# Kernel optimization log

Measured on AMD Instinct MI355X. Metric: run time of the kernel, lower is better.

## Reference

```python
import jax, jax.numpy as jnp
import numpy as np

D_MODEL = 1024
NUM_HEADS = 16
HEAD_DIM = D_MODEL // NUM_HEADS
SEQ_LEN = 2048
BATCH = 2


def setup_inputs() -> dict:
    key = jax.random.key(0)
    ks = jax.random.split(key, 8)
    s = 1.0 / np.sqrt(D_MODEL)
    x = jax.random.normal(ks[0], (BATCH, SEQ_LEN, D_MODEL), jnp.float32)
    Wq = jax.random.normal(ks[1], (D_MODEL, D_MODEL), jnp.float32) * s
    Wk = jax.random.normal(ks[2], (D_MODEL, D_MODEL), jnp.float32) * s
    Wv = jax.random.normal(ks[3], (D_MODEL, D_MODEL), jnp.float32) * s
    Wo = jax.random.normal(ks[4], (D_MODEL, D_MODEL), jnp.float32) * s
    bq = jnp.zeros((D_MODEL,), jnp.float32)
    bk = jnp.zeros((D_MODEL,), jnp.float32)
    bv = jnp.zeros((D_MODEL,), jnp.float32)
    bo = jnp.zeros((D_MODEL,), jnp.float32)
    pos_embed = jax.random.normal(ks[5], (SEQ_LEN, HEAD_DIM), jnp.float32) * (1.0 / np.sqrt(HEAD_DIM))
    alpha = jnp.ones((NUM_HEADS, 1, 1), jnp.float32)
    beta = jnp.zeros((NUM_HEADS, 1, 1), jnp.float32)
    mask = jnp.ones((BATCH, SEQ_LEN), jnp.int32)
    return {"x": x, "mask": mask, "Wq": Wq, "bq": bq, "Wk": Wk, "bk": bk,
            "Wv": Wv, "bv": bv, "Wo": Wo, "bo": bo,
            "pos_embed": pos_embed, "alpha": alpha, "beta": beta}


def reference(x, mask, Wq, bq, Wk, bk, Wv, bv, Wo, bo, pos_embed, alpha, beta):
    B, S, _ = x.shape
    H, Dh = NUM_HEADS, HEAD_DIM
    # projections (torch Linear: x @ W^T + b), reshape to [B,H,S,Dh]
    def proj(W, b):
        return (x @ W.T + b).reshape(B, S, H, Dh).transpose(0, 2, 1, 3)
    q = proj(Wq, bq)
    k = proj(Wk, bk)
    v = proj(Wv, bv)
    # content scores [B,H,S,S]
    content = jnp.einsum('bhqd,bhkd->bhqk', q, k) / np.sqrt(Dh).astype(np.float32)
    # position scores [S,S] -> broadcast; combined with per-head alpha/beta
    pe = pos_embed[:S]
    pos_attn = pe @ pe.T  # [S,S]
    scores = content + (alpha * pos_attn[None] + beta)[None]  # [B,H,S,S]
    # mask: [B,S] broadcast over heads and query positions (key-side mask)
    scores = jnp.where(mask[:, None, None, :] == 0, -jnp.inf, scores)
    probs = jax.nn.softmax(scores, axis=-1)
    out = jnp.einsum('bhqk,bhkd->bhqd', probs, v)  # [B,H,S,Dh]
    out = out.transpose(0, 2, 1, 3).reshape(B, S, H * Dh)
    return out @ Wo.T + bo
```

## Files before the change

kernel.cpp:

```cpp
#include <hip/hip_runtime.h>

#define BATCH 2
#define SEQ   2048
#define NH    16
#define DH    64
#define DA    128
#define DM    1024
#define MTOT  (BATCH*SEQ)

typedef _Float16 f16x8 __attribute__((ext_vector_type(8)));
typedef _Float16 f16x4 __attribute__((ext_vector_type(4)));
typedef float    f32x4 __attribute__((ext_vector_type(4)));
typedef float    f32x16 __attribute__((ext_vector_type(16)));

#define LOG2E 1.44269504088896340736f

#define OFF_X16 0u
#define OFF_WQ  8388608u
#define OFF_WK  10485760u
#define OFF_WV  12582912u
#define OFF_WO  14680064u
#define OFF_QA  16777216u
#define OFF_KA  33554432u
#define OFF_VT  50331648u
#define OFF_AO  58720256u

__device__ __forceinline__ void gload_lds16(const _Float16* g, _Float16* l) {
  __builtin_amdgcn_global_load_lds(
      (const __attribute__((address_space(1))) unsigned int*)g,
      (__attribute__((address_space(3))) unsigned int*)l, 16, 0, 0);
}

__device__ __forceinline__ float fexp2(float x) {
  float r;
  asm("v_exp_f32 %0, %1" : "=v"(r) : "v"(x));
  return r;
}

__device__ __forceinline__ unsigned pk2(float a, float b) {
  auto v = __builtin_amdgcn_cvt_pkrtz(a, b);
  return *(unsigned*)&v;
}

__global__ __launch_bounds__(256) void prep(
    const float* __restrict__ x,  const float* __restrict__ wq,
    const float* __restrict__ wk, const float* __restrict__ wv,
    const float* __restrict__ wo, _Float16* __restrict__ dst,
    const float* __restrict__ pe, const float* __restrict__ alpha,
    _Float16* __restrict__ Qa, _Float16* __restrict__ Ka)
{
  int bid = blockIdx.x;
  if (bid < 4096) {
    int i = bid * 256 + threadIdx.x;
    const float* src;
    if (i < 524288) {
      src = x + (size_t)i * 8;
    } else {
      int j = i - 524288;
      int wi = j >> 17;
      const float* w = (wi == 0) ? wq : ((wi == 1) ? wk : ((wi == 2) ? wv : wo));
      src = w + (size_t)(j & 131071) * 8;
    }
    float4 a = ((const float4*)src)[0];
    float4 c = ((const float4*)src)[1];
    f16x8 hv;
    hv[0]=(_Float16)a.x; hv[1]=(_Float16)a.y; hv[2]=(_Float16)a.z; hv[3]=(_Float16)a.w;
    hv[4]=(_Float16)c.x; hv[5]=(_Float16)c.y; hv[6]=(_Float16)c.z; hv[7]=(_Float16)c.w;
    *(f16x8*)(dst + (size_t)i * 8) = hv;
  } else {
    int idx = (bid - 4096) * 256 + threadIdx.x;
    int c8 = idx & 7;
    int s  = (idx >> 3) & 2047;
    int h  = (idx >> 14) & 15;
    int b  = idx >> 18;
    const float4* p4 = (const float4*)(pe + s * 64 + c8 * 8);
    float4 a = p4[0], c = p4[1];
    float al = alpha[h] * LOG2E;
    f16x8 hk, hq;
    hk[0]=(_Float16)a.x; hk[1]=(_Float16)a.y; hk[2]=(_Float16)a.z; hk[3]=(_Float16)a.w;
    hk[4]=(_Float16)c.x; hk[5]=(_Float16)c.y; hk[6]=(_Float16)c.z; hk[7]=(_Float16)c.w;
    hq[0]=(_Float16)(al*a.x); hq[1]=(_Float16)(al*a.y); hq[2]=(_Float16)(al*a.z); hq[3]=(_Float16)(al*a.w);
    hq[4]=(_Float16)(al*c.x); hq[5]=(_Float16)(al*c.y); hq[6]=(_Float16)(al*c.z); hq[7]=(_Float16)(al*c.w);
    size_t o = ((size_t)((b * NH + h) * SEQ + s)) * DA + 64 + c8 * 8;
    *(f16x8*)&Qa[o] = hq;
    *(f16x8*)&Ka[o] = hk;
  }
}

template<int MODE>
__global__ __launch_bounds__(512) void gemm_nt(
    const _Float16* __restrict__ A,
    const _Float16* __restrict__ W0, const _Float16* __restrict__ W1,
    const _Float16* __restrict__ W2,
    const float* __restrict__ b0, const float* __restrict__ b1,
    const float* __restrict__ b2,
    _Float16* __restrict__ Qa, _Float16* __restrict__ Ka,
    _Float16* __restrict__ Vt, float* __restrict__ Out)
{
  __shared__ _Float16 As[128 * 64];
  __shared__ _Float16 Bs[128 * 64];
  const int tid = threadIdx.x;
  const int w = tid >> 6, lane = tid & 63;
  const int g = lane >> 4, l16 = lane & 15;
  const int wm = w >> 2, wn = w & 3;

  int nb_all = blockIdx.x;
  int mblk = blockIdx.y;
  const _Float16* Bp; const float* biasp;
  int which = 0, nblk = nb_all;
  if (MODE == 0) {
    which = nb_all >> 3; nblk = nb_all & 7;
    Bp = (which == 0) ? W0 : ((which == 1) ? W1 : W2);
    biasp = (which == 0) ? b0 : ((which == 1) ? b1 : b2);
  } else {
    Bp = W0; biasp = b0;
  }

  f32x4 zero4 = {0.f, 0.f, 0.f, 0.f};
  f32x4 acc[4][2];
  #pragma unroll
  for (int mb = 0; mb < 4; ++mb)
    #pragma unroll
    for (int nb = 0; nb < 2; ++nb) acc[mb][nb] = zero4;

  const _Float16* Abase = A  + (size_t)mblk * 128 * DM;
  const _Float16* Bbase = Bp + (size_t)nblk * 128 * DM;

  for (int kt = 0; kt < DM / 64; ++kt) {
    __syncthreads();
    #pragma unroll
    for (int ii = 0; ii < 2; ++ii) {
      int i = w * 2 + ii;
      int rt = i * 8 + (lane >> 3);
      int cg = (lane & 7) ^ (rt & 7);
      gload_lds16(Abase + (size_t)rt * DM + kt * 64 + cg * 8, &As[i * 512]);
    }
    #pragma unroll
    for (int ii = 0; ii < 2; ++ii) {
      int i = w * 2 + ii;
      int rt = i * 8 + (lane >> 3);
      int cg = (lane & 7) ^ (rt & 7);
      gload_lds16(Bbase + (size_t)rt * DM + kt * 64 + cg * 8, &Bs[i * 512]);
    }
    __syncthreads();
    #pragma unroll
    for (int ks = 0; ks < 2; ++ks) {
      f16x8 av[4], bv[2];
      #pragma unroll
      for (int mb = 0; mb < 4; ++mb) {
        int rt = wm * 64 + mb * 16 + l16;
        av[mb] = *(const f16x8*)&As[rt * 64 + (((ks * 4 + g) ^ (rt & 7)) * 8)];
      }
      #pragma unroll
      for (int nb = 0; nb < 2; ++nb) {
        int rt = wn * 32 + nb * 16 + l16;
        bv[nb] = *(const f16x8*)&Bs[rt * 64 + (((ks * 4 + g) ^ (rt & 7)) * 8)];
      }
      #pragma unroll
      for (int mb = 0; mb < 4; ++mb)
        #pragma unroll
        for (int nb = 0; nb < 2; ++nb)
          acc[mb][nb] = __builtin_amdgcn_mfma_f32_16x16x32_f16(
              av[mb], bv[nb], acc[mb][nb], 0, 0, 0);
    }
  }

  #pragma unroll
  for (int nb = 0; nb < 2; ++nb) {
    int n = nblk * 128 + wn * 32 + nb * 16 + l16;
    float bias = biasp[n];
    #pragma unroll
    for (int mb = 0; mb < 4; ++mb) {
      int m0 = mblk * 128 + wm * 64 + mb * 16 + g * 4;
      if (MODE == 0) {
        int hh = n >> 6, dd = n & 63;
        if (which == 2) {
          int bb = m0 >> 11, ss = m0 & 2047;
          f16x4 hv;
          #pragma unroll
          for (int r = 0; r < 4; ++r) hv[r] = (_Float16)(acc[mb][nb][r] + bias);
          *(f16x4*)&Vt[((size_t)((bb * NH + hh) * DH + dd)) * SEQ + ss] = hv;
        } else {
          #pragma unroll
          for (int r = 0; r < 4; ++r) {
            int m = m0 + r; int bb = m >> 11, ss = m & 2047;
            size_t o = ((size_t)((bb * NH + hh) * SEQ + ss)) * DA + dd;
            if (which == 0) Qa[o] = (_Float16)((acc[mb][nb][r] + bias) * (0.125f * LOG2E));
            else            Ka[o] = (_Float16)(acc[mb][nb][r] + bias);
          }
        }
      } else {
        #pragma unroll
        for (int r = 0; r < 4; ++r)
          Out[(size_t)(m0 + r) * DM + n] = acc[mb][nb][r] + bias;
      }
    }
  }
}

__global__ __launch_bounds__(256, 3) void flash_attn(
    const _Float16* __restrict__ Qa, const _Float16* __restrict__ Ka,
    const _Float16* __restrict__ Vt, const int* __restrict__ mask,
    _Float16* __restrict__ AO)
{
  __shared__ _Float16 Ks[2][64 * 128];
  __shared__ _Float16 Vs[2][64 * 64];
  const int tid = threadIdx.x;
  const int w = tid >> 6, lane = tid & 63;
  const int l32 = lane & 31, hi = lane >> 5;

  int bid = blockIdx.x;
  int work = (bid & 7) * 64 + (bid >> 3);
  const int qt = work & 15;
  const int bh = work >> 4;
  const int h = bh & 15, b = bh >> 4;

  const _Float16* qbase = Qa + ((size_t)(bh * SEQ) + qt * 128 + w * 32) * DA;
  f16x8 qf[8];
  #pragma unroll
  for (int c16 = 0; c16 < 8; ++c16)
    qf[c16] = *(const f16x8*)&qbase[l32 * DA + c16 * 16 + hi * 8];

  f32x16 acco[2];
  #pragma unroll
  for (int db = 0; db < 2; ++db)
    #pragma unroll
    for (int r = 0; r < 16; ++r) acco[db][r] = 0.f;
  float mrun = -3.0e38f, lrun = 0.f;

  const _Float16* kbase = Ka + (size_t)bh * SEQ * DA;
  const _Float16* vbase = Vt + (size_t)bh * DH * SEQ;
  const int* mbase = mask + b * SEQ;

  int allm = 1;
  #pragma unroll 8
  for (int t = 0; t < SEQ / 64; ++t) allm &= (mbase[t * 64 + lane] != 0);
  const bool maskclean = __all(allm);

  auto STAGE = [&](int buf, int kt) {
    #pragma unroll
    for (int ii = 0; ii < 4; ++ii) {
      int i = ii * 256 + tid;
      int rt = i >> 4, c = i & 15;
      int cg = c ^ (rt & 7);
      gload_lds16(kbase + (size_t)(kt * 64 + rt) * DA + cg * 8, &Ks[buf][i * 8]);
    }
    #pragma unroll
    for (int ii = 0; ii < 2; ++ii) {
      int i = ii * 256 + tid;
      int rt = i >> 3, c = i & 7;
      int cg = c ^ (rt & 7);
      gload_lds16(vbase + (size_t)rt * SEQ + kt * 64 + cg * 8, &Vs[buf][i * 8]);
    }
  };

  STAGE(0, 0);
  int cur = 0;
  for (int kt = 0; kt < SEQ / 64; ++kt) {
    asm volatile("s_waitcnt lgkmcnt(0)" ::: "memory");
    __builtin_amdgcn_s_barrier();
    asm volatile("" ::: "memory");
    if (kt + 1 < SEQ / 64) {
      STAGE(cur ^ 1, kt + 1);
      asm volatile("s_waitcnt vmcnt(6)" ::: "memory");
    } else {
      asm volatile("s_waitcnt vmcnt(0)" ::: "memory");
    }
    __builtin_amdgcn_s_barrier();
    asm volatile("" ::: "memory");

    f32x16 sfr[2];
    __builtin_amdgcn_s_setprio(1);
    #pragma unroll
    for (int kb = 0; kb < 2; ++kb) {
      f32x16 s;
      #pragma unroll
      for (int r = 0; r < 16; ++r) s[r] = 0.f;
      int rt = kb * 32 + l32;
      #pragma unroll
      for (int c16 = 0; c16 < 8; ++c16) {
        int ch = (2 * c16 + hi) ^ (rt & 7);
        f16x8 kf = *(const f16x8*)&Ks[cur][rt * 128 + ch * 8];
        s = __builtin_amdgcn_mfma_f32_32x32x16_f16(kf, qf[c16], s, 0, 0, 0);
      }
      sfr[kb] = s;
    }
    __builtin_amdgcn_s_setprio(0);

    if (!maskclean) {
      #pragma unroll
      for (int kb = 0; kb < 2; ++kb)
        #pragma unroll
        for (int r = 0; r < 16; ++r) {
          int key = kt * 64 + kb * 32 + (r & 3) + 8 * (r >> 2) + 4 * hi;
          if (mbase[key] == 0) sfr[kb][r] = -3.0e38f;
        }
    }

    float mx = sfr[0][0];
    #pragma unroll
    for (int kb = 0; kb < 2; ++kb)
      #pragma unroll
      for (int r = 0; r < 16; ++r) mx = fmaxf(mx, sfr[kb][r]);
    mx = fmaxf(mx, __shfl_xor(mx, 32));

    const bool rescale = !__all(mx <= mrun + 8.0f);
    float mnew = mrun, scale = 1.0f;
    if (rescale) {
      mnew = fmaxf(mrun, mx);
      scale = fexp2(mrun - mnew);
    }
    float rsum = 0.f;
    unsigned pk[2][4][2];
    #pragma unroll
    for (int kb = 0; kb < 2; ++kb)
      #pragma unroll
      for (int rq = 0; rq < 4; ++rq) {
        float p0 = fexp2(sfr[kb][rq * 4 + 0] - mnew);
        float p1 = fexp2(sfr[kb][rq * 4 + 1] - mnew);
        float p2 = fexp2(sfr[kb][rq * 4 + 2] - mnew);
        float p3 = fexp2(sfr[kb][rq * 4 + 3] - mnew);
        rsum += (p0 + p1) + (p2 + p3);
        pk[kb][rq][0] = pk2(p0, p1);
        pk[kb][rq][1] = pk2(p2, p3);
      }
    rsum += __shfl_xor(rsum, 32);
    if (rescale) {
      lrun = lrun * scale + rsum;
      mrun = mnew;
      #pragma unroll
      for (int db = 0; db < 2; ++db)
        #pragma unroll
        for (int r = 0; r < 16; ++r) acco[db][r] *= scale;
    } else {
      lrun += rsum;
    }

    __builtin_amdgcn_s_setprio(1);
    #pragma unroll
    for (int c = 0; c < 4; ++c) {
      const int kb = c >> 1, c2 = c & 1;
      unsigned X0 = pk[kb][2 * c2][0],     X1 = pk[kb][2 * c2][1];
      unsigned Y0 = pk[kb][2 * c2 + 1][0], Y1 = pk[kb][2 * c2 + 1][1];
      asm("v_permlane32_swap_b32 %0, %1" : "+v"(X0), "+v"(Y0));
      asm("v_permlane32_swap_b32 %0, %1" : "+v"(X1), "+v"(Y1));
      union { unsigned u[4]; f16x8 v; } pu;
      pu.u[0] = X0; pu.u[1] = X1; pu.u[2] = Y0; pu.u[3] = Y1;
      #pragma unroll
      for (int db = 0; db < 2; ++db) {
        int row = db * 32 + l32;
        int ch = (2 * c + hi) ^ (row & 7);
        f16x8 vf = *(const f16x8*)&Vs[cur][row * 64 + ch * 8];
        acco[db] = __builtin_amdgcn_mfma_f32_32x32x16_f16(vf, pu.v, acco[db], 0, 0, 0);
      }
    }
    __builtin_amdgcn_s_setprio(0);
    cur ^= 1;
  }

  float inv = 1.0f / lrun;
  int sg = qt * 128 + w * 32 + l32;
  _Float16* aobase = AO + ((size_t)(b * SEQ + sg)) * DM + h * DH;
  #pragma unroll
  for (int db = 0; db < 2; ++db)
    #pragma unroll
    for (int rq = 0; rq < 4; ++rq) {
      f16x4 o;
      #pragma unroll
      for (int j = 0; j < 4; ++j) o[j] = (_Float16)(acco[db][rq * 4 + j] * inv);
      *(f16x4*)&aobase[db * 32 + rq * 8 + hi * 4] = o;
    }
}

extern "C" void kernel_launch(void* const* d_in, const int* in_sizes, int n_in,
                              void* d_out, int out_size, void* d_ws, size_t ws_size,
                              hipStream_t stream) {
  const float* x     = (const float*)d_in[0];
  const int*   mask  = (const int*)  d_in[1];
  const float* Wq    = (const float*)d_in[2];
  const float* bq    = (const float*)d_in[3];
  const float* Wk    = (const float*)d_in[4];
  const float* bk    = (const float*)d_in[5];
  const float* Wv    = (const float*)d_in[6];
  const float* bv    = (const float*)d_in[7];
  const float* Wo    = (const float*)d_in[8];
  const float* bo    = (const float*)d_in[9];
  const float* pe    = (const float*)d_in[10];
  const float* alpha = (const float*)d_in[11];

  char* ws = (char*)d_ws;
  _Float16* x16 = (_Float16*)(ws + OFF_X16);
  _Float16* wq6 = (_Float16*)(ws + OFF_WQ);
  _Float16* wk6 = (_Float16*)(ws + OFF_WK);
  _Float16* wv6 = (_Float16*)(ws + OFF_WV);
  _Float16* wo6 = (_Float16*)(ws + OFF_WO);
  _Float16* Qa  = (_Float16*)(ws + OFF_QA);
  _Float16* Ka  = (_Float16*)(ws + OFF_KA);
  _Float16* Vt  = (_Float16*)(ws + OFF_VT);
  _Float16* AO  = (_Float16*)(ws + OFF_AO);
  float* out = (float*)d_out;

  prep<<<6144, 256, 0, stream>>>(x, Wq, Wk, Wv, Wo, x16, pe, alpha, Qa, Ka);
  gemm_nt<0><<<dim3(24, 32), 512, 0, stream>>>(x16, wq6, wk6, wv6, bq, bk, bv,
                                               Qa, Ka, Vt, nullptr);
  flash_attn<<<512, 256, 0, stream>>>(Qa, Ka, Vt, mask, AO);
  gemm_nt<1><<<dim3(8, 32), 512, 0, stream>>>(AO, wo6, nullptr, nullptr, bo,
                                              nullptr, nullptr, nullptr, nullptr,
                                              nullptr, out);
}
```

Before: 130.1 us.

## Split KV range across two wave groups and double queries per wave in flash attention

```diff
diff --git a/kernel.cpp b/kernel.cpp
--- a/kernel.cpp
+++ b/kernel.cpp
@@ -198,69 +198,78 @@
   }
 }
 
-__global__ __launch_bounds__(256, 3) void flash_attn(
+__global__ __launch_bounds__(512, 2) void flash_attn(
     const _Float16* __restrict__ Qa, const _Float16* __restrict__ Ka,
     const _Float16* __restrict__ Vt, const int* __restrict__ mask,
     _Float16* __restrict__ AO)
 {
-  __shared__ _Float16 Ks[2][64 * 128];
-  __shared__ _Float16 Vs[2][64 * 64];
+  __shared__ char smem[98304];
+  _Float16* KsP = (_Float16*)smem;
+  _Float16* VsP = (_Float16*)(smem + 65536);
   const int tid = threadIdx.x;
   const int w = tid >> 6, lane = tid & 63;
   const int l32 = lane & 31, hi = lane >> 5;
+  const int half = w >> 2, wsub = w & 3;
 
   int bid = blockIdx.x;
-  int work = (bid & 7) * 64 + (bid >> 3);
-  const int qt = work & 15;
-  const int bh = work >> 4;
+  int work = (bid & 7) * 32 + (bid >> 3);
+  const int qt = work & 7;
+  const int bh = work >> 3;
   const int h = bh & 15, b = bh >> 4;
 
-  const _Float16* qbase = Qa + ((size_t)(bh * SEQ) + qt * 128 + w * 32) * DA;
-  f16x8 qf[8];
+  const _Float16* qbase = Qa + ((size_t)(bh * SEQ) + qt * 256 + wsub * 64) * DA;
+  f16x8 qf[2][8];
   #pragma unroll
-  for (int c16 = 0; c16 < 8; ++c16)
-    qf[c16] = *(const f16x8*)&qbase[l32 * DA + c16 * 16 + hi * 8];
-
-  f32x16 acco[2];
+  for (int qs = 0; qs < 2; ++qs)
+    #pragma unroll
+    for (int c16 = 0; c16 < 8; ++c16)
+      qf[qs][c16] = *(const f16x8*)&qbase[(qs * 32 + l32) * DA + c16 * 16 + hi * 8];
+
+  f32x16 acco[2][2];
   #pragma unroll
   for (int db = 0; db < 2; ++db)
     #pragma unroll
-    for (int r = 0; r < 16; ++r) acco[db][r] = 0.f;
-  float mrun = -3.0e38f, lrun = 0.f;
-
-  const _Float16* kbase = Ka + (size_t)bh * SEQ * DA;
-  const _Float16* vbase = Vt + (size_t)bh * DH * SEQ;
-  const int* mbase = mask + b * SEQ;
+    for (int qs = 0; qs < 2; ++qs)
+      #pragma unroll
+      for (int r = 0; r < 16; ++r) acco[db][qs][r] = 0.f;
+  float mrun[2] = {-3.0e38f, -3.0e38f}, lrun[2] = {0.f, 0.f};
+
+  const _Float16* kbaseh = Ka + (size_t)bh * SEQ * DA + (size_t)(half * 1024) * DA;
+  const _Float16* vbaseh = Vt + (size_t)bh * DH * SEQ + half * 1024;
+  const int* mbaseh = mask + b * SEQ + half * 1024;
 
   int allm = 1;
   #pragma unroll 8
-  for (int t = 0; t < SEQ / 64; ++t) allm &= (mbase[t * 64 + lane] != 0);
+  for (int t = 0; t < 16; ++t) allm &= (mbaseh[t * 64 + lane] != 0);
   const bool maskclean = __all(allm);
 
   auto STAGE = [&](int buf, int kt) {
+    _Float16* kd = KsP + (half * 2 + buf) * 8192;
+    _Float16* vd = VsP + (half * 2 + buf) * 4096;
+    int t = tid & 255;
     #pragma unroll
     for (int ii = 0; ii < 4; ++ii) {
-      int i = ii * 256 + tid;
+      int i = ii * 256 + t;
       int rt = i >> 4, c = i & 15;
       int cg = c ^ (rt & 7);
-      gload_lds16(kbase + (size_t)(kt * 64 + rt) * DA + cg * 8, &Ks[buf][i * 8]);
+      gload_lds16(kbaseh + (size_t)(kt * 64 + rt) * DA + cg * 8, kd + i * 8);
     }
     #pragma unroll
     for (int ii = 0; ii < 2; ++ii) {
-      int i = ii * 256 + tid;
+      int i = ii * 256 + t;
       int rt = i >> 3, c = i & 7;
       int cg = c ^ (rt & 7);
-      gload_lds16(vbase + (size_t)rt * SEQ + kt * 64 + cg * 8, &Vs[buf][i * 8]);
+      gload_lds16(vbaseh + (size_t)rt * SEQ + kt * 64 + cg * 8, vd + i * 8);
     }
   };
 
   STAGE(0, 0);
   int cur = 0;
-  for (int kt = 0; kt < SEQ / 64; ++kt) {
+  for (int kt = 0; kt < 16; ++kt) {
     asm volatile("s_waitcnt lgkmcnt(0)" ::: "memory");
     __builtin_amdgcn_s_barrier();
     asm volatile("" ::: "memory");
-    if (kt + 1 < SEQ / 64) {
+    if (kt + 1 < 16) {
       STAGE(cur ^ 1, kt + 1);
       asm volatile("s_waitcnt vmcnt(6)" ::: "memory");
     } else {
@@ -269,21 +278,25 @@
     __builtin_amdgcn_s_barrier();
     asm volatile("" ::: "memory");
 
-    f32x16 sfr[2];
+    const _Float16* kd = KsP + (half * 2 + cur) * 8192;
+    const _Float16* vd = VsP + (half * 2 + cur) * 4096;
+
+    f32x16 sfr[2][2];
     __builtin_amdgcn_s_setprio(1);
     #pragma unroll
     for (int kb = 0; kb < 2; ++kb) {
-      f32x16 s;
-      #pragma unroll
-      for (int r = 0; r < 16; ++r) s[r] = 0.f;
+      f32x16 s0, s1;
+      #pragma unroll
+      for (int r = 0; r < 16; ++r) { s0[r] = 0.f; s1[r] = 0.f; }
       int rt = kb * 32 + l32;
       #pragma unroll
       for (int c16 = 0; c16 < 8; ++c16) {
         int ch = (2 * c16 + hi) ^ (rt & 7);
-        f16x8 kf = *(const f16x8*)&Ks[cur][rt * 128 + ch * 8];
-        s = __builtin_amdgcn_mfma_f32_32x32x16_f16(kf, qf[c16], s, 0, 0, 0);
-      }
-      sfr[kb] = s;
+        f16x8 kf = *(const f16x8*)&kd[rt * 128 + ch * 8];
+        s0 = __builtin_amdgcn_mfma_f32_32x32x16_f16(kf, qf[0][c16], s0, 0, 0, 0);
+        s1 = __builtin_amdgcn_mfma_f32_32x32x16_f16(kf, qf[1][c16], s1, 0, 0, 0);
+      }
+      sfr[kb][0] = s0; sfr[kb][1] = s1;
     }
     __builtin_amdgcn_s_setprio(0);
 
@@ -293,83 +306,141 @@
         #pragma unroll
         for (int r = 0; r < 16; ++r) {
           int key = kt * 64 + kb * 32 + (r & 3) + 8 * (r >> 2) + 4 * hi;
-          if (mbase[key] == 0) sfr[kb][r] = -3.0e38f;
+          if (mbaseh[key] == 0) { sfr[kb][0][r] = -3.0e38f; sfr[kb][1][r] = -3.0e38f; }
         }
     }
 
-    float mx = sfr[0][0];
-    #pragma unroll
-    for (int kb = 0; kb < 2; ++kb)
-      #pragma unroll
-      for (int r = 0; r < 16; ++r) mx = fmaxf(mx, sfr[kb][r]);
-    mx = fmaxf(mx, __shfl_xor(mx, 32));
-
-    const bool rescale = !__all(mx <= mrun + 8.0f);
-    float mnew = mrun, scale = 1.0f;
-    if (rescale) {
-      mnew = fmaxf(mrun, mx);
-      scale = fexp2(mrun - mnew);
-    }
-    float rsum = 0.f;
-    unsigned pk[2][4][2];
-    #pragma unroll
-    for (int kb = 0; kb < 2; ++kb)
-      #pragma unroll
-      for (int rq = 0; rq < 4; ++rq) {
-        float p0 = fexp2(sfr[kb][rq * 4 + 0] - mnew);
-        float p1 = fexp2(sfr[kb][rq * 4 + 1] - mnew);
-        float p2 = fexp2(sfr[kb][rq * 4 + 2] - mnew);
-        float p3 = fexp2(sfr[kb][rq * 4 + 3] - mnew);
-        rsum += (p0 + p1) + (p2 + p3);
-        pk[kb][rq][0] = pk2(p0, p1);
-        pk[kb][rq][1] = pk2(p2, p3);
-      }
-    rsum += __shfl_xor(rsum, 32);
-    if (rescale) {
-      lrun = lrun * scale + rsum;
-      mrun = mnew;
-      #pragma unroll
-      for (int db = 0; db < 2; ++db)
-        #pragma unroll
-        for (int r = 0; r < 16; ++r) acco[db][r] *= scale;
-    } else {
-      lrun += rsum;
+    unsigned pk[2][2][4][2];
+    #pragma unroll
+    for (int qs = 0; qs < 2; ++qs) {
+      float mx = sfr[0][qs][0];
+      #pragma unroll
+      for (int kb = 0; kb < 2; ++kb)
+        #pragma unroll
+        for (int r = 0; r < 16; ++r) mx = fmaxf(mx, sfr[kb][qs][r]);
+      mx = fmaxf(mx, __shfl_xor(mx, 32));
+
+      const bool rescale = !__all(mx <= mrun[qs] + 8.0f);
+      float mnew = mrun[qs], scale = 1.0f;
+      if (rescale) {
+        mnew = fmaxf(mrun[qs], mx);
+        scale = fexp2(mrun[qs] - mnew);
+      }
+      float rsum = 0.f;
+      #pragma unroll
+      for (int kb = 0; kb < 2; ++kb)
+        #pragma unroll
+        for (int rq = 0; rq < 4; ++rq) {
+          float p0 = fexp2(sfr[kb][qs][rq * 4 + 0] - mnew);
+          float p1 = fexp2(sfr[kb][qs][rq * 4 + 1] - mnew);
+          float p2 = fexp2(sfr[kb][qs][rq * 4 + 2] - mnew);
+          float p3 = fexp2(sfr[kb][qs][rq * 4 + 3] - mnew);
+          rsum += (p0 + p1) + (p2 + p3);
+          pk[qs][kb][rq][0] = pk2(p0, p1);
+          pk[qs][kb][rq][1] = pk2(p2, p3);
+        }
+      rsum += __shfl_xor(rsum, 32);
+      if (rescale) {
+        lrun[qs] = lrun[qs] * scale + rsum;
+        mrun[qs] = mnew;
+        #pragma unroll
+        for (int db = 0; db < 2; ++db)
+          #pragma unroll
+          for (int r = 0; r < 16; ++r) acco[db][qs][r] *= scale;
+      } else {
+        lrun[qs] += rsum;
+      }
     }
 
     __builtin_amdgcn_s_setprio(1);
     #pragma unroll
     for (int c = 0; c < 4; ++c) {
       const int kb = c >> 1, c2 = c & 1;
-      unsigned X0 = pk[kb][2 * c2][0],     X1 = pk[kb][2 * c2][1];
-      unsigned Y0 = pk[kb][2 * c2 + 1][0], Y1 = pk[kb][2 * c2 + 1][1];
-      asm("v_permlane32_swap_b32 %0, %1" : "+v"(X0), "+v"(Y0));
-      asm("v_permlane32_swap_b32 %0, %1" : "+v"(X1), "+v"(Y1));
-      union { unsigned u[4]; f16x8 v; } pu;
-      pu.u[0] = X0; pu.u[1] = X1; pu.u[2] = Y0; pu.u[3] = Y1;
+      union { unsigned u[4]; f16x8 v; } pu0, pu1;
+      {
+        unsigned X0 = pk[0][kb][2 * c2][0],     X1 = pk[0][kb][2 * c2][1];
+        unsigned Y0 = pk[0][kb][2 * c2 + 1][0], Y1 = pk[0][kb][2 * c2 + 1][1];
+        asm("v_permlane32_swap_b32 %0, %1" : "+v"(X0), "+v"(Y0));
+        asm("v_permlane32_swap_b32 %0, %1" : "+v"(X1), "+v"(Y1));
+        pu0.u[0] = X0; pu0.u[1] = X1; pu0.u[2] = Y0; pu0.u[3] = Y1;
+      }
+      {
+        unsigned X0 = pk[1][kb][2 * c2][0],     X1 = pk[1][kb][2 * c2][1];
+        unsigned Y0 = pk[1][kb][2 * c2 + 1][0], Y1 = pk[1][kb][2 * c2 + 1][1];
+        asm("v_permlane32_swap_b32 %0, %1" : "+v"(X0), "+v"(Y0));
+        asm("v_permlane32_swap_b32 %0, %1" : "+v"(X1), "+v"(Y1));
+        pu1.u[0] = X0; pu1.u[1] = X1; pu1.u[2] = Y0; pu1.u[3] = Y1;
+      }
       #pragma unroll
       for (int db = 0; db < 2; ++db) {
         int row = db * 32 + l32;
         int ch = (2 * c + hi) ^ (row & 7);
-        f16x8 vf = *(const f16x8*)&Vs[cur][row * 64 + ch * 8];
-        acco[db] = __builtin_amdgcn_mfma_f32_32x32x16_f16(vf, pu.v, acco[db], 0, 0, 0);
+        f16x8 vf = *(const f16x8*)&vd[row * 64 + ch * 8];
+        acco[db][0] = __builtin_amdgcn_mfma_f32_32x32x16_f16(vf, pu0.v, acco[db][0], 0, 0, 0);
+        acco[db][1] = __builtin_amdgcn_mfma_f32_32x32x16_f16(vf, pu1.v, acco[db][1], 0, 0, 0);
       }
     }
     __builtin_amdgcn_s_setprio(0);
     cur ^= 1;
   }
 
-  float inv = 1.0f / lrun;
-  int sg = qt * 128 + w * 32 + l32;
-  _Float16* aobase = AO + ((size_t)(b * SEQ + sg)) * DM + h * DH;
-  #pragma unroll
-  for (int db = 0; db < 2; ++db)
-    #pragma unroll
-    for (int rq = 0; rq < 4; ++rq) {
-      f16x4 o;
-      #pragma unroll
-      for (int j = 0; j < 4; ++j) o[j] = (_Float16)(acco[db][rq * 4 + j] * inv);
-      *(f16x4*)&aobase[db * 32 + rq * 8 + hi * 4] = o;
-    }
+  __syncthreads();
+  float* cacc = (float*)smem;
+  float4* cml = (float4*)(smem + 65536);
+  if (half == 1) {
+    #pragma unroll
+    for (int db = 0; db < 2; ++db)
+      #pragma unroll
+      for (int qs = 0; qs < 2; ++qs)
+        #pragma unroll
+        for (int rq = 0; rq < 4; ++rq) {
+          int cc = (db * 2 + qs) * 4 + rq;
+          float4 v4;
+          v4.x = acco[db][qs][rq * 4 + 0]; v4.y = acco[db][qs][rq * 4 + 1];
+          v4.z = acco[db][qs][rq * 4 + 2]; v4.w = acco[db][qs][rq * 4 + 3];
+          *(float4*)&cacc[((wsub * 16 + cc) * 64 + lane) * 4] = v4;
+        }
+    float4 mlv;
+    mlv.x = mrun[0]; mlv.y = lrun[0]; mlv.z = mrun[1]; mlv.w = lrun[1];
+    cml[wsub * 64 + lane] = mlv;
+  }
+  __syncthreads();
+  if (half == 0) {
+    float4 mlv = cml[wsub * 64 + lane];
+    float w0q[2], w1q[2], linv[2];
+    {
+      float m1 = mlv.x, l1 = mlv.y;
+      float m = fmaxf(mrun[0], m1);
+      w0q[0] = fexp2(mrun[0] - m); w1q[0] = fexp2(m1 - m);
+      float l = lrun[0] * w0q[0] + l1 * w1q[0];
+      linv[0] = (l > 0.f) ? (1.0f / l) : 0.f;
+    }
+    {
+      float m1 = mlv.z, l1 = mlv.w;
+      float m = fmaxf(mrun[1], m1);
+      w0q[1] = fexp2(mrun[1] - m); w1q[1] = fexp2(m1 - m);
+      float l = lrun[1] * w0q[1] + l1 * w1q[1];
+      linv[1] = (l > 0.f) ? (1.0f / l) : 0.f;
+    }
+    #pragma unroll
+    for (int qs = 0; qs < 2; ++qs) {
+      int sg = qt * 256 + wsub * 64 + qs * 32 + l32;
+      _Float16* aobase = AO + ((size_t)(b * SEQ + sg)) * DM + h * DH;
+      #pragma unroll
+      for (int db = 0; db < 2; ++db)
+        #pragma unroll
+        for (int rq = 0; rq < 4; ++rq) {
+          int cc = (db * 2 + qs) * 4 + rq;
+          float4 p4 = *(const float4*)&cacc[((wsub * 16 + cc) * 64 + lane) * 4];
+          f16x4 o;
+          o[0] = (_Float16)((acco[db][qs][rq * 4 + 0] * w0q[qs] + p4.x * w1q[qs]) * linv[qs]);
+          o[1] = (_Float16)((acco[db][qs][rq * 4 + 1] * w0q[qs] + p4.y * w1q[qs]) * linv[qs]);
+          o[2] = (_Float16)((acco[db][qs][rq * 4 + 2] * w0q[qs] + p4.z * w1q[qs]) * linv[qs]);
+          o[3] = (_Float16)((acco[db][qs][rq * 4 + 3] * w0q[qs] + p4.w * w1q[qs]) * linv[qs]);
+          *(f16x4*)&aobase[db * 32 + rq * 8 + hi * 4] = o;
+        }
+    }
+  }
 }
 
 extern "C" void kernel_launch(void* const* d_in, const int* in_sizes, int n_in,
@@ -403,7 +474,7 @@
   prep<<<6144, 256, 0, stream>>>(x, Wq, Wk, Wv, Wo, x16, pe, alpha, Qa, Ka);
   gemm_nt<0><<<dim3(24, 32), 512, 0, stream>>>(x16, wq6, wk6, wv6, bq, bk, bv,
                                                Qa, Ka, Vt, nullptr);
-  flash_attn<<<512, 256, 0, stream>>>(Qa, Ka, Vt, mask, AO);
+  flash_attn<<<256, 512, 0, stream>>>(Qa, Ka, Vt, mask, AO);
   gemm_nt<1><<<dim3(8, 32), 512, 0, stream>>>(AO, wo6, nullptr, nullptr, bo,
                                               nullptr, nullptr, nullptr, nullptr,
                                               nullptr, out);
```

Result: no change. 128.3 us (-1.4%).

## Remap GEMM blocks per XCD, unroll attention loop by two, tree-reduce max/sum

Applied to the files above, without the earlier changes.

```diff
diff --git a/kernel.cpp b/kernel.cpp
--- a/kernel.cpp
+++ b/kernel.cpp
@@ -104,8 +104,12 @@
   const int g = lane >> 4, l16 = lane & 15;
   const int wm = w >> 2, wn = w & 3;
 
-  int nb_all = blockIdx.x;
-  int mblk = blockIdx.y;
+  int lin = blockIdx.x;
+  int xcd = lin & 7, j = lin >> 3;
+  int mblk, nb_all;
+  if (MODE == 0) { mblk = (xcd & 3) * 8 + (j & 7); nb_all = (xcd >> 2) * 12 + (j >> 3); }
+  else           { mblk = xcd * 4 + (j & 3);       nb_all = j >> 2; }
+
   const _Float16* Bp; const float* biasp;
   int which = 0, nblk = nb_all;
   if (MODE == 0) {
@@ -254,14 +258,12 @@
     }
   };
 
-  STAGE(0, 0);
-  int cur = 0;
-  for (int kt = 0; kt < SEQ / 64; ++kt) {
+  auto TILE = [&](int kt, int buf) {
     asm volatile("s_waitcnt lgkmcnt(0)" ::: "memory");
     __builtin_amdgcn_s_barrier();
     asm volatile("" ::: "memory");
     if (kt + 1 < SEQ / 64) {
-      STAGE(cur ^ 1, kt + 1);
+      STAGE(buf ^ 1, kt + 1);
       asm volatile("s_waitcnt vmcnt(6)" ::: "memory");
     } else {
       asm volatile("s_waitcnt vmcnt(0)" ::: "memory");
@@ -280,7 +282,7 @@
       #pragma unroll
       for (int c16 = 0; c16 < 8; ++c16) {
         int ch = (2 * c16 + hi) ^ (rt & 7);
-        f16x8 kf = *(const f16x8*)&Ks[cur][rt * 128 + ch * 8];
+        f16x8 kf = *(const f16x8*)&Ks[buf][rt * 128 + ch * 8];
         s = __builtin_amdgcn_mfma_f32_32x32x16_f16(kf, qf[c16], s, 0, 0, 0);
       }
       sfr[kb] = s;
@@ -297,12 +299,14 @@
         }
     }
 
-    float mx = sfr[0][0];
-    #pragma unroll
-    for (int kb = 0; kb < 2; ++kb)
-      #pragma unroll
-      for (int r = 0; r < 16; ++r) mx = fmaxf(mx, sfr[kb][r]);
-    mx = fmaxf(mx, __shfl_xor(mx, 32));
+    float mtree[16];
+    #pragma unroll
+    for (int r = 0; r < 16; ++r) mtree[r] = fmaxf(sfr[0][r], sfr[1][r]);
+    #pragma unroll
+    for (int st = 8; st > 0; st >>= 1)
+      #pragma unroll
+      for (int r = 0; r < st; ++r) mtree[r] = fmaxf(mtree[r], mtree[r + st]);
+    float mx = fmaxf(mtree[0], __shfl_xor(mtree[0], 32));
 
     const bool rescale = !__all(mx <= mrun + 8.0f);
     float mnew = mrun, scale = 1.0f;
@@ -310,8 +314,8 @@
       mnew = fmaxf(mrun, mx);
       scale = fexp2(mrun - mnew);
     }
-    float rsum = 0.f;
     unsigned pk[2][4][2];
+    float gsum[8];
     #pragma unroll
     for (int kb = 0; kb < 2; ++kb)
       #pragma unroll
@@ -320,11 +324,15 @@
         float p1 = fexp2(sfr[kb][rq * 4 + 1] - mnew);
         float p2 = fexp2(sfr[kb][rq * 4 + 2] - mnew);
         float p3 = fexp2(sfr[kb][rq * 4 + 3] - mnew);
-        rsum += (p0 + p1) + (p2 + p3);
+        gsum[kb * 4 + rq] = (p0 + p1) + (p2 + p3);
         pk[kb][rq][0] = pk2(p0, p1);
         pk[kb][rq][1] = pk2(p2, p3);
       }
-    rsum += __shfl_xor(rsum, 32);
+    #pragma unroll
+    for (int st = 4; st > 0; st >>= 1)
+      #pragma unroll
+      for (int r = 0; r < st; ++r) gsum[r] += gsum[r + st];
+    float rsum = gsum[0] + __shfl_xor(gsum[0], 32);
     if (rescale) {
       lrun = lrun * scale + rsum;
       mrun = mnew;
@@ -350,12 +358,17 @@
       for (int db = 0; db < 2; ++db) {
         int row = db * 32 + l32;
         int ch = (2 * c + hi) ^ (row & 7);
-        f16x8 vf = *(const f16x8*)&Vs[cur][row * 64 + ch * 8];
+        f16x8 vf = *(const f16x8*)&Vs[buf][row * 64 + ch * 8];
         acco[db] = __builtin_amdgcn_mfma_f32_32x32x16_f16(vf, pu.v, acco[db], 0, 0, 0);
       }
     }
     __builtin_amdgcn_s_setprio(0);
-    cur ^= 1;
+  };
+
+  STAGE(0, 0);
+  for (int kt = 0; kt < SEQ / 64; kt += 2) {
+    TILE(kt, 0);
+    TILE(kt + 1, 1);
   }
 
   float inv = 1.0f / lrun;
@@ -401,10 +414,10 @@
   float* out = (float*)d_out;
 
   prep<<<6144, 256, 0, stream>>>(x, Wq, Wk, Wv, Wo, x16, pe, alpha, Qa, Ka);
-  gemm_nt<0><<<dim3(24, 32), 512, 0, stream>>>(x16, wq6, wk6, wv6, bq, bk, bv,
-                                               Qa, Ka, Vt, nullptr);
+  gemm_nt<0><<<768, 512, 0, stream>>>(x16, wq6, wk6, wv6, bq, bk, bv,
+                                      Qa, Ka, Vt, nullptr);
   flash_attn<<<512, 256, 0, stream>>>(Qa, Ka, Vt, mask, AO);
-  gemm_nt<1><<<dim3(8, 32), 512, 0, stream>>>(AO, wo6, nullptr, nullptr, bo,
-                                              nullptr, nullptr, nullptr, nullptr,
-                                              nullptr, out);
-}
+  gemm_nt<1><<<256, 512, 0, stream>>>(AO, wo6, nullptr, nullptr, bo,
+                                      nullptr, nullptr, nullptr, nullptr,
+                                      nullptr, out);
+}
```

Result: no change. 130.6 us (+0.4%).
